# Performance work log

Measured on AMD Instinct MI355X. Metric: run time of the kernel, lower is better.

The kernel has to match this reference:

```python
import jax, jax.numpy as jnp
import numpy as np

N_NODES = 100000
N_EDGES = 1600000
HID = 64
EDGE_DIM = 16
SC_DIM = 6  # max_cycle(8) - MIN_CYCLE(3) + 1
N_LAYERS = 2
MSG_IN = 2 * HID + 2 * SC_DIM + EDGE_DIM  # 156
UPD_IN = 2 * HID


def setup_inputs() -> dict:
    key = jax.random.key(0)
    ks = jax.random.split(key, 16)
    s = 0.05
    inp = {
        "x": jax.random.normal(ks[0], (N_NODES, HID), dtype=jnp.float32),
        "edge_list": jax.random.randint(ks[1], (N_EDGES, 2), 0, N_NODES, dtype=jnp.int32),
        "node_struct": jax.random.randint(ks[2], (N_NODES, SC_DIM), 0, 4, dtype=jnp.int32),
        "edge_feature": jax.random.normal(ks[3], (N_EDGES, EDGE_DIM), dtype=jnp.float32),
        "edge_weight": jnp.ones((N_EDGES,), dtype=jnp.float32),
        "node2graph": jnp.sort(jax.random.randint(ks[4], (N_NODES,), 0, 128, dtype=jnp.int32)),
        "num_graphs": 128,
        # params
        "lin_w": jax.random.normal(ks[5], (HID, HID), dtype=jnp.float32) * s,
        "lin_b": jnp.zeros((HID,), dtype=jnp.float32),
        "msg_w1": jax.random.normal(ks[6], (N_LAYERS, MSG_IN, HID), dtype=jnp.float32) * s,
        "msg_b1": jnp.zeros((N_LAYERS, HID), dtype=jnp.float32),
        "msg_w2": jax.random.normal(ks[7], (N_LAYERS, HID, HID), dtype=jnp.float32) * s,
        "msg_b2": jnp.zeros((N_LAYERS, HID), dtype=jnp.float32),
        "upd_w1": jax.random.normal(ks[8], (N_LAYERS, UPD_IN, HID), dtype=jnp.float32) * s,
        "upd_b1": jnp.zeros((N_LAYERS, HID), dtype=jnp.float32),
        "upd_w2": jax.random.normal(ks[9], (N_LAYERS, HID, HID), dtype=jnp.float32) * s,
        "upd_b2": jnp.zeros((N_LAYERS, HID), dtype=jnp.float32),
    }
    return inp


def reference(x, edge_list, node_struct, edge_feature, edge_weight, node2graph,
              num_graphs, lin_w, lin_b, msg_w1, msg_b1, msg_w2, msg_b2,
              upd_w1, upd_b1, upd_w2, upd_b2):
    n_node = x.shape[0]
    src = edge_list[:, 0]
    dst = edge_list[:, 1]
    sc = node_struct.astype(x.dtype)          # [N, 6] structural cycle counts
    h = x @ lin_w + lin_b                      # input projection [N, HID]
    for l in range(N_LAYERS):
        # message: gather endpoints + structural feats + edge feats, 2-layer MLP
        m = jnp.concatenate([h[src], h[dst], sc[src], sc[dst], edge_feature], axis=-1)
        m = jax.nn.relu(m @ msg_w1[l] + msg_b1[l]) @ msg_w2[l] + msg_b2[l]
        # aggregate: weighted scatter_add onto destination nodes
        upd = jax.ops.segment_sum(m * edge_weight[:, None], dst, num_segments=n_node)
        # combine: cat(input, update) -> 2-layer MLP -> outer activation
        z = jnp.concatenate([h, upd], axis=-1)
        z = jax.nn.relu(z @ upd_w1[l] + upd_b1[l]) @ upd_w2[l] + upd_b2[l]
        h = jax.nn.relu(z)
    node_feature = h
    graph_feature = jax.ops.segment_sum(node_feature, node2graph, num_segments=num_graphs)
    return graph_feature, node_feature
```

## Files before the change

### kernel.cpp

```cpp
#include <hip/hip_runtime.h>

#define NN 100000
#define NE 1600000
#define HID 64
#define MSG_IN 156
#define W1E_OFF 140

__device__ __forceinline__ void mm4x4(float (&acc)[4][4], const float4 a, const float4 b) {
    acc[0][0] = fmaf(a.x, b.x, acc[0][0]);
    acc[0][1] = fmaf(a.x, b.y, acc[0][1]);
    acc[0][2] = fmaf(a.x, b.z, acc[0][2]);
    acc[0][3] = fmaf(a.x, b.w, acc[0][3]);
    acc[1][0] = fmaf(a.y, b.x, acc[1][0]);
    acc[1][1] = fmaf(a.y, b.y, acc[1][1]);
    acc[1][2] = fmaf(a.y, b.z, acc[1][2]);
    acc[1][3] = fmaf(a.y, b.w, acc[1][3]);
    acc[2][0] = fmaf(a.z, b.x, acc[2][0]);
    acc[2][1] = fmaf(a.z, b.y, acc[2][1]);
    acc[2][2] = fmaf(a.z, b.z, acc[2][2]);
    acc[2][3] = fmaf(a.z, b.w, acc[2][3]);
    acc[3][0] = fmaf(a.w, b.x, acc[3][0]);
    acc[3][1] = fmaf(a.w, b.y, acc[3][1]);
    acc[3][2] = fmaf(a.w, b.z, acc[3][2]);
    acc[3][3] = fmaf(a.w, b.w, acc[3][3]);
}


__global__ __launch_bounds__(256) void k_sw(
    const int2* __restrict__ el2, const float* __restrict__ ew,
    float* __restrict__ sw, int n_edges)
{
    int e = blockIdx.x * 256 + threadIdx.x;
    if (e < n_edges) atomicAdd(&sw[el2[e].y], ew[e]);
}

__global__ __launch_bounds__(256) void k_hist2(
    const int2* __restrict__ el2, const float* __restrict__ ew,
    int* __restrict__ counts, float* __restrict__ sw, int n_edges)
{
    int e = blockIdx.x * 256 + threadIdx.x;
    if (e < n_edges) {
        int2 sd = el2[e];
        atomicAdd(&counts[sd.y], 1);
        atomicAdd(&sw[sd.y], ew[e]);
    }
}

__global__ __launch_bounds__(256) void k_scan1(
    const int* counts, int* offs, int* __restrict__ blksum, int n)
{
    __shared__ int s[256];
    const int tid = threadIdx.x;
    int i = blockIdx.x * 256 + tid;
    int v = (i < n) ? counts[i] : 0;
    s[tid] = v;
    for (int off = 1; off < 256; off <<= 1) {
        __syncthreads();
        int t = (tid >= off) ? s[tid - off] : 0;
        __syncthreads();
        s[tid] += t;
    }
    __syncthreads();
    if (i < n) offs[i] = s[tid] - v;
    if (tid == 255) blksum[blockIdx.x] = s[255];
}

__global__ __launch_bounds__(512) void k_scan2(int* __restrict__ blksum, int nb)
{
    __shared__ int s[512];
    const int tid = threadIdx.x;
    int v = (tid < nb) ? blksum[tid] : 0;
    s[tid] = v;
    for (int off = 1; off < 512; off <<= 1) {
        __syncthreads();
        int t = (tid >= off) ? s[tid - off] : 0;
        __syncthreads();
        s[tid] += t;
    }
    __syncthreads();
    if (tid < nb) blksum[tid] = s[tid] - v;
}

__global__ __launch_bounds__(256) void k_scan3(
    int* __restrict__ offs, const int* __restrict__ blksum, int n)
{
    int i = blockIdx.x * 256 + threadIdx.x;
    if (i < n) offs[i] += blksum[blockIdx.x];
}

__global__ __launch_bounds__(256) void k_permute(
    const int2* __restrict__ el2, int* __restrict__ cursor,
    int* __restrict__ perm, int n_edges)
{
    int e = blockIdx.x * 256 + threadIdx.x;
    if (e < n_edges) {
        int pos = atomicAdd(&cursor[el2[e].y], 1);
        perm[pos] = e;
    }
}

__global__ __launch_bounds__(256) void k_csmall(
    const float* __restrict__ msg_w2, const float* __restrict__ upd_w1,
    const float* __restrict__ msg_b2, float* __restrict__ C2, float* __restrict__ db2)
{
    const int l = blockIdx.x;
    const float* W2  = msg_w2 + (size_t)l * 4096;
    const float* U1b = upd_w1 + (size_t)l * 8192 + 4096;
    const float* b2  = msg_b2 + l * 64;
    float* C  = C2  + (size_t)l * 4096;
    float* db = db2 + l * 64;
    __shared__ __align__(16) float At[64][68];
    __shared__ __align__(16) float B[64][64];
    const int tid = threadIdx.x;
    for (int i = tid; i < 1024; i += 256) {
        ((float4*)B)[i] = ((const float4*)U1b)[i];
        int m = i >> 4, f4 = i & 15, k4 = f4 * 4;
        float4 v = ((const float4*)W2)[m * 16 + f4];
        At[k4 + 0][m] = v.x; At[k4 + 1][m] = v.y; At[k4 + 2][m] = v.z; At[k4 + 3][m] = v.w;
    }
    __syncthreads();
    const int ty = tid >> 4, tx = tid & 15;
    float acc[4][4];
    #pragma unroll
    for (int r = 0; r < 4; ++r) { acc[r][0]=0.f; acc[r][1]=0.f; acc[r][2]=0.f; acc[r][3]=0.f; }
    #pragma unroll 8
    for (int k = 0; k < 64; ++k) {
        float4 a = *(const float4*)&At[k][ty * 4];
        float4 bv = *(const float4*)&B[k][tx * 4];
        mm4x4(acc, a, bv);
    }
    #pragma unroll
    for (int r = 0; r < 4; ++r)
        ((float4*)C)[(ty * 4 + r) * 16 + tx] = make_float4(acc[r][0], acc[r][1], acc[r][2], acc[r][3]);
    if (tid < 64) {
        float sum = 0.f;
        for (int k = 0; k < 64; ++k) sum += b2[k] * B[k][tid];
        db[tid] = sum;
    }
}


__global__ __launch_bounds__(256) void k_init(
    const float* __restrict__ x, const float* __restrict__ w,
    const float* __restrict__ b, float* __restrict__ h, int n)
{
    __shared__ __align__(16) float At[64][68];
    __shared__ __align__(16) float B[64][64];
    const int tid = threadIdx.x;
    const int m0 = blockIdx.x * 64;
    for (int i = tid; i < 1024; i += 256)
        ((float4*)B)[i] = ((const float4*)w)[i];
    for (int i = tid; i < 1024; i += 256) {
        int m = i >> 4, f4 = i & 15, k4 = f4 * 4;
        int node = m0 + m;
        float4 v = make_float4(0.f, 0.f, 0.f, 0.f);
        if (node < n) v = ((const float4*)x)[node * 16 + f4];
        At[k4 + 0][m] = v.x; At[k4 + 1][m] = v.y; At[k4 + 2][m] = v.z; At[k4 + 3][m] = v.w;
    }
    __syncthreads();
    const int ty = tid >> 4, tx = tid & 15;
    float acc[4][4];
    {
        float4 bb = ((const float4*)b)[tx];
        #pragma unroll
        for (int r = 0; r < 4; ++r) { acc[r][0]=bb.x; acc[r][1]=bb.y; acc[r][2]=bb.z; acc[r][3]=bb.w; }
    }
    #pragma unroll 8
    for (int k = 0; k < 64; ++k) {
        float4 a = *(const float4*)&At[k][ty * 4];
        float4 bv = *(const float4*)&B[k][tx * 4];
        mm4x4(acc, a, bv);
    }
    #pragma unroll
    for (int r = 0; r < 4; ++r) {
        int node = m0 + ty * 4 + r;
        if (node < n)
            ((float4*)h)[node * 16 + tx] = make_float4(acc[r][0], acc[r][1], acc[r][2], acc[r][3]);
    }
}

__global__ __launch_bounds__(256) void k_pq(
    const float* __restrict__ h, const int* __restrict__ nsc,
    const float* __restrict__ w1, const float* __restrict__ b1,
    float* __restrict__ p, float* __restrict__ q, int n)
{
    __shared__ __align__(16) float At[64][68];
    __shared__ __align__(16) float Bp[64][64];
    __shared__ __align__(16) float Bq[64][64];
    __shared__ __align__(16) float Sct[6][68];
    __shared__ __align__(16) float Bc[6][64];
    __shared__ __align__(16) float Bd[6][64];
    const int tid = threadIdx.x;
    const int m0 = blockIdx.x * 64;
    for (int i = tid; i < 1024; i += 256) {
        ((float4*)Bp)[i] = ((const float4*)w1)[i];
        ((float4*)Bq)[i] = ((const float4*)(w1 + 64 * 64))[i];
    }
    if (tid < 96) {
        ((float4*)Bc)[tid] = ((const float4*)(w1 + 128 * 64))[tid];
        ((float4*)Bd)[tid] = ((const float4*)(w1 + 134 * 64))[tid];
    }
    for (int i = tid; i < 1024; i += 256) {
        int m = i >> 4, f4 = i & 15, k4 = f4 * 4;
        int node = m0 + m;
        float4 v = make_float4(0.f, 0.f, 0.f, 0.f);
        if (node < n) v = ((const float4*)h)[node * 16 + f4];
        At[k4 + 0][m] = v.x; At[k4 + 1][m] = v.y; At[k4 + 2][m] = v.z; At[k4 + 3][m] = v.w;
    }
    for (int i = tid; i < 384; i += 256) {
        int m = i & 63, k = i >> 6;
        int node = m0 + m;
        float v = 0.f;
        if (node < n) v = (float)nsc[node * 6 + k];
        Sct[k][m] = v;
    }
    __syncthreads();
    const int ty = tid >> 4, tx = tid & 15;
    float ap[4][4], aq[4][4];
    {
        float4 bb = ((const float4*)b1)[tx];
        #pragma unroll
        for (int r = 0; r < 4; ++r) {
            ap[r][0]=0.f; ap[r][1]=0.f; ap[r][2]=0.f; ap[r][3]=0.f;
            aq[r][0]=bb.x; aq[r][1]=bb.y; aq[r][2]=bb.z; aq[r][3]=bb.w;
        }
    }
    #pragma unroll 8
    for (int k = 0; k < 64; ++k) {
        float4 a  = *(const float4*)&At[k][ty * 4];
        float4 bp = *(const float4*)&Bp[k][tx * 4];
        float4 bq = *(const float4*)&Bq[k][tx * 4];
        mm4x4(ap, a, bp);
        mm4x4(aq, a, bq);
    }
    #pragma unroll
    for (int k = 0; k < 6; ++k) {
        float4 a  = *(const float4*)&Sct[k][ty * 4];
        float4 bc = *(const float4*)&Bc[k][tx * 4];
        float4 bd = *(const float4*)&Bd[k][tx * 4];
        mm4x4(ap, a, bc);
        mm4x4(aq, a, bd);
    }
    #pragma unroll
    for (int r = 0; r < 4; ++r) {
        int node = m0 + ty * 4 + r;
        if (node < n) {
            ((float4*)p)[node * 16 + tx] = make_float4(ap[r][0], ap[r][1], ap[r][2], ap[r][3]);
            ((float4*)q)[node * 16 + tx] = make_float4(aq[r][0], aq[r][1], aq[r][2], aq[r][3]);
        }
    }
}


struct Meta { int pe[4]; };
struct El   { int s[4]; int d[4]; float w[4]; };
struct Pv   { float4 pv[4]; };
struct Run  { int d; float s0, s1, s2, s3; };

__device__ __forceinline__ void load_perm(Meta& m, int& spe, int c0, int eEnd,
    int ty, int tid, const int* __restrict__ perm)
{
    #pragma unroll
    for (int r = 0; r < 4; ++r) {
        int e = c0 + ty * 4 + r;
        m.pe[r] = perm[e < eEnd ? e : (eEnd - 1)];
    }
    int es = c0 + (tid >> 2);
    spe = perm[es < eEnd ? es : (eEnd - 1)];
}

__device__ __forceinline__ void load_el(El& e, const Meta& m,
    const int2* __restrict__ el2, const float* __restrict__ ew)
{
    #pragma unroll
    for (int r = 0; r < 4; ++r) {
        int2 sd = el2[m.pe[r]];
        e.s[r] = sd.x; e.d[r] = sd.y; e.w[r] = ew[m.pe[r]];
    }
}

__device__ __forceinline__ void load_p(Pv& z, const El& e,
    const float4* __restrict__ p4, int tx)
{
    #pragma unroll
    for (int r = 0; r < 4; ++r)
        z.pv[r] = p4[(size_t)e.s[r] * 16 + tx];
}

__device__ __forceinline__ void stage_ef(float (*Eb)[68], float4 v, int tid)
{
    int e = tid >> 2, k4 = (tid & 3) * 4;
    Eb[k4 + 0][e] = v.x; Eb[k4 + 1][e] = v.y;
    Eb[k4 + 2][e] = v.z; Eb[k4 + 3][e] = v.w;
}

__device__ __forceinline__ void flush_run(float (*Sacc)[68], const Run& run,
    int d0, int tx)
{
    float* dp = &Sacc[run.d - d0][tx * 4];
    atomicAdd(dp + 0, run.s0); atomicAdd(dp + 1, run.s1);
    atomicAdd(dp + 2, run.s2); atomicAdd(dp + 3, run.s3);
}

__device__ __forceinline__ void compute_chunk(const El& el, const Pv& pvr,
    int c0, int eEnd, int d0, const float (*Eb)[68], const float (*W1e)[64],
    float (*Sacc)[68], const float4* __restrict__ q4, int ty, int tx, Run& run)
{
    float4 qv[4];
    #pragma unroll
    for (int r = 0; r < 4; ++r)
        qv[r] = q4[(size_t)el.d[r] * 16 + tx];
    float acc[4][4];
    #pragma unroll
    for (int r = 0; r < 4; ++r) {
        acc[r][0] = pvr.pv[r].x; acc[r][1] = pvr.pv[r].y;
        acc[r][2] = pvr.pv[r].z; acc[r][3] = pvr.pv[r].w;
    }
    #pragma unroll
    for (int k = 0; k < 16; ++k) {
        float4 a = *(const float4*)&Eb[k][ty * 4];
        float4 bv = *(const float4*)&W1e[k][tx * 4];
        mm4x4(acc, a, bv);
    }
    #pragma unroll
    for (int r = 0; r < 4; ++r) {
        acc[r][0] += qv[r].x; acc[r][1] += qv[r].y;
        acc[r][2] += qv[r].z; acc[r][3] += qv[r].w;
    }
    #pragma unroll
    for (int r = 0; r < 4; ++r) {
        bool act = (c0 + ty * 4 + r) < eEnd;
        float w = act ? el.w[r] : 0.f;
        int d = el.d[r];
        float v0 = fmaxf(acc[r][0], 0.f) * w;
        float v1 = fmaxf(acc[r][1], 0.f) * w;
        float v2 = fmaxf(acc[r][2], 0.f) * w;
        float v3 = fmaxf(acc[r][3], 0.f) * w;
        if (d != run.d) {
            if (run.d >= 0) flush_run(Sacc, run, d0, tx);
            run.d = d; run.s0 = v0; run.s1 = v1; run.s2 = v2; run.s3 = v3;
        } else {
            run.s0 += v0; run.s1 += v1; run.s2 += v2; run.s3 += v3;
        }
    }
}

__device__ __forceinline__ void step(int c0, int eEnd, int d0, int& buf,
    Meta& mX, int& speX, El& elX, Pv& pvX,
    Meta& mY, int& speY, El& elY, Pv& pvY,
    const int* __restrict__ perm, const int2* __restrict__ el2,
    const float* __restrict__ ew, const float4* __restrict__ ef4,
    const float4* __restrict__ p4, const float4* __restrict__ q4,
    float (*Et)[16][68], const float (*W1e)[64], float (*Sacc)[68],
    int tid, int ty, int tx, Run& run)
{
    float4 efv = ef4[(size_t)speY * 4 + (tid & 3)];
    load_p(pvY, elY, p4, tx);
    load_perm(mX, speX, c0 + 128, eEnd, ty, tid, perm);
    compute_chunk(elX, pvX, c0, eEnd, d0, Et[buf], W1e, Sacc, q4, ty, tx, run);
    load_el(elX, mX, el2, ew);
    stage_ef(Et[buf ^ 1], efv, tid);
    __syncthreads();
    buf ^= 1;
}

__global__ __launch_bounds__(256) void k_edge5(
    const int* __restrict__ perm, const int* __restrict__ ends,
    const int2* __restrict__ el2, const float* __restrict__ ew,
    const float* __restrict__ ef,
    const float* __restrict__ p, const float* __restrict__ q,
    const float* __restrict__ w1e, float* __restrict__ S, int n_nodes)
{
    __shared__ __align__(16) float W1e[16][64];
    __shared__ __align__(16) float Sacc[64][68];
    __shared__ __align__(16) float Et[2][16][68];
    const int tid = threadIdx.x;
    int b = blockIdx.x;
    {
        const int nb = gridDim.x;
        const int qn = nb >> 3, rr = nb & 7;
        const int xcd = b & 7, idx = b >> 3;
        b = (xcd < rr ? xcd * (qn + 1) : rr * (qn + 1) + (xcd - rr) * qn) + idx;
    }
    const int d0 = b * 64;
    const int dn = min(64, n_nodes - d0);
    const int eStart = (d0 == 0) ? 0 : ends[d0 - 1];
    const int eEnd   = ends[d0 + dn - 1];
    const int nc = (eEnd - eStart + 63) >> 6;

    const float4* p4  = (const float4*)p;
    const float4* q4  = (const float4*)q;
    const float4* ef4 = (const float4*)ef;

    ((float4*)W1e)[tid] = ((const float4*)w1e)[tid];
    for (int i = tid; i < 64 * 17; i += 256)
        ((float4*)Sacc)[i] = make_float4(0.f, 0.f, 0.f, 0.f);

    const int ty = tid >> 4, tx = tid & 15;
    Run run; run.d = -1; run.s0 = run.s1 = run.s2 = run.s3 = 0.f;

    if (nc > 0) {
        Meta mX, mY; int speX, speY;
        El elX, elY;
        Pv pvX, pvY;
        load_perm(mX, speX, eStart, eEnd, ty, tid, perm);
        load_el(elX, mX, el2, ew);
        float4 ef0 = ef4[(size_t)speX * 4 + (tid & 3)];
        load_p(pvX, elX, p4, tx);
        load_perm(mY, speY, eStart + 64, eEnd, ty, tid, perm);
        load_el(elY, mY, el2, ew);
        stage_ef(Et[0], ef0, tid);
        __syncthreads();

        int buf = 0;
        for (int c = 0; c < nc; c += 2) {
            step(eStart + (c << 6), eEnd, d0, buf,
                 mX, speX, elX, pvX, mY, speY, elY, pvY,
                 perm, el2, ew, ef4, p4, q4, Et, W1e, Sacc, tid, ty, tx, run);
            if (c + 1 < nc)
                step(eStart + ((c + 1) << 6), eEnd, d0, buf,
                     mY, speY, elY, pvY, mX, speX, elX, pvX,
                     perm, el2, ew, ef4, p4, q4, Et, W1e, Sacc, tid, ty, tx, run);
        }
    }
    if (run.d >= 0) flush_run(Sacc, run, d0, tx);
    __syncthreads();
    for (int i = tid; i < dn * 16; i += 256) {
        int row = i >> 4, f4 = i & 15;
        ((float4*)S)[(size_t)(d0 + row) * 16 + f4] = *(const float4*)&Sacc[row][f4 * 4];
    }
}

__global__ __launch_bounds__(256) void k_edge2(
    const int* __restrict__ perm, const int2* __restrict__ el2,
    const float* __restrict__ ew, const float* __restrict__ ef,
    const float* __restrict__ p, const float* __restrict__ q,
    const float* __restrict__ w1e, float* __restrict__ S, int n_edges)
{
    __shared__ __align__(16) float Et[16][68];
    __shared__ __align__(16) float W1e[16][64];
    __shared__ int Ssrc[64];
    __shared__ int Sdst[64];
    __shared__ float Sew[64];
    const int tid = threadIdx.x;
    const int b = blockIdx.x, nb = gridDim.x;
    const int tile = ((nb & 7) == 0) ? ((b & 7) * (nb >> 3) + (b >> 3)) : b;
    const int e0 = tile * 64;
    if (tid < 64) {
        int e = e0 + tid;
        int s = 0, d = 0; float w = 0.f;
        if (e < n_edges) {
            int pe = perm ? perm[e] : e;
            int2 sd = el2[pe];
            s = sd.x; d = sd.y; w = ew[pe];
        }
        Ssrc[tid] = s; Sdst[tid] = d; Sew[tid] = w;
    }
    ((float4*)W1e)[tid] = ((const float4*)w1e)[tid];
    {
        int e = tid >> 2, f4 = tid & 3, k4 = f4 * 4;
        int ge = e0 + e;
        float4 v = make_float4(0.f, 0.f, 0.f, 0.f);
        if (ge < n_edges) {
            int pe = perm ? perm[ge] : ge;
            v = ((const float4*)ef)[(size_t)pe * 4 + f4];
        }
        Et[k4 + 0][e] = v.x; Et[k4 + 1][e] = v.y; Et[k4 + 2][e] = v.z; Et[k4 + 3][e] = v.w;
    }
    __syncthreads();
    const int ty = tid >> 4, tx = tid & 15;
    float acc[4][4];
    #pragma unroll
    for (int r = 0; r < 4; ++r) {
        int s = Ssrc[ty * 4 + r], d = Sdst[ty * 4 + r];
        float4 pv = ((const float4*)p)[(size_t)s * 16 + tx];
        float4 qv = ((const float4*)q)[(size_t)d * 16 + tx];
        acc[r][0] = pv.x + qv.x; acc[r][1] = pv.y + qv.y;
        acc[r][2] = pv.z + qv.z; acc[r][3] = pv.w + qv.w;
    }
    #pragma unroll
    for (int k = 0; k < 16; ++k) {
        float4 a = *(const float4*)&Et[k][ty * 4];
        float4 bv = *(const float4*)&W1e[k][tx * 4];
        mm4x4(acc, a, bv);
    }
    {
        int curd = -1;
        float s0 = 0.f, s1 = 0.f, s2 = 0.f, s3 = 0.f;
        #pragma unroll
        for (int r = 0; r < 4; ++r) {
            int le = ty * 4 + r;
            int ge = e0 + le;
            if (ge < n_edges) {
                int d = Sdst[le];
                float w = Sew[le];
                float v0 = fmaxf(acc[r][0], 0.f) * w;
                float v1 = fmaxf(acc[r][1], 0.f) * w;
                float v2 = fmaxf(acc[r][2], 0.f) * w;
                float v3 = fmaxf(acc[r][3], 0.f) * w;
                if (d != curd) {
                    if (curd >= 0) {
                        atomicAdd(&S[(size_t)curd * 64 + tx * 4 + 0], s0);
                        atomicAdd(&S[(size_t)curd * 64 + tx * 4 + 1], s1);
                        atomicAdd(&S[(size_t)curd * 64 + tx * 4 + 2], s2);
                        atomicAdd(&S[(size_t)curd * 64 + tx * 4 + 3], s3);
                    }
                    curd = d; s0 = v0; s1 = v1; s2 = v2; s3 = v3;
                } else {
                    s0 += v0; s1 += v1; s2 += v2; s3 += v3;
                }
            }
        }
        if (curd >= 0) {
            atomicAdd(&S[(size_t)curd * 64 + tx * 4 + 0], s0);
            atomicAdd(&S[(size_t)curd * 64 + tx * 4 + 1], s1);
            atomicAdd(&S[(size_t)curd * 64 + tx * 4 + 2], s2);
            atomicAdd(&S[(size_t)curd * 64 + tx * 4 + 3], s3);
        }
    }
}

__global__ __launch_bounds__(256) void k_update(
    float* __restrict__ h, const float* __restrict__ S,
    const float* __restrict__ w1, const float* __restrict__ C,
    const float* __restrict__ b1, const float* __restrict__ w2,
    const float* __restrict__ b2, const float* __restrict__ db,
    const float* __restrict__ sw,
    int n, int write_out, float* __restrict__ out_graph,
    const int* __restrict__ n2g)
{
    __shared__ __align__(16) float At[64][68];
    __shared__ __align__(16) float B1[128][64];
    __shared__ float Db[64];
    const int tid = threadIdx.x;
    const int m0 = blockIdx.x * 64;
    const int ty = tid >> 4, tx = tid & 15;
    if (tid < 64) Db[tid] = db[tid];
    for (int i = tid; i < 2048; i += 256)
        ((float4*)B1)[i] = (i < 1024) ? ((const float4*)w1)[i] : ((const float4*)C)[i - 1024];
    for (int i = tid; i < 1024; i += 256) {
        int m = i >> 4, f4 = i & 15, k4 = f4 * 4;
        int node = m0 + m;
        float4 v = make_float4(0.f, 0.f, 0.f, 0.f);
        if (node < n) v = ((const float4*)h)[node * 16 + f4];
        At[k4 + 0][m] = v.x; At[k4 + 1][m] = v.y; At[k4 + 2][m] = v.z; At[k4 + 3][m] = v.w;
    }
    __syncthreads();
    float acc[4][4];
    {
        float4 bb = ((const float4*)b1)[tx];
        #pragma unroll
        for (int r = 0; r < 4; ++r) { acc[r][0]=bb.x; acc[r][1]=bb.y; acc[r][2]=bb.z; acc[r][3]=bb.w; }
    }
    #pragma unroll 8
    for (int k = 0; k < 64; ++k) {
        float4 a = *(const float4*)&At[k][ty * 4];
        float4 bv = *(const float4*)&B1[k][tx * 4];
        mm4x4(acc, a, bv);
    }
    __syncthreads();
    for (int i = tid; i < 1024; i += 256) {
        int m = i >> 4, f4 = i & 15, k4 = f4 * 4;
        int node = m0 + m;
        float4 v = make_float4(0.f, 0.f, 0.f, 0.f);
        if (node < n) v = ((const float4*)S)[node * 16 + f4];
        At[k4 + 0][m] = v.x; At[k4 + 1][m] = v.y; At[k4 + 2][m] = v.z; At[k4 + 3][m] = v.w;
    }
    __syncthreads();
    #pragma unroll 8
    for (int k = 0; k < 64; ++k) {
        float4 a = *(const float4*)&At[k][ty * 4];
        float4 bv = *(const float4*)&B1[64 + k][tx * 4];
        mm4x4(acc, a, bv);
    }
    #pragma unroll
    for (int r = 0; r < 4; ++r) {
        int node = m0 + ty * 4 + r;
        float swv = (node < n) ? sw[node] : 0.f;
        #pragma unroll
        for (int c = 0; c < 4; ++c)
            acc[r][c] = fmaf(swv, Db[tx * 4 + c], acc[r][c]);
    }
    __syncthreads();
    #pragma unroll
    for (int r = 0; r < 4; ++r)
        #pragma unroll
        for (int c = 0; c < 4; ++c)
            At[tx * 4 + c][ty * 4 + r] = fmaxf(acc[r][c], 0.f);
    for (int i = tid; i < 1024; i += 256)
        ((float4*)B1)[i] = ((const float4*)w2)[i];
    __syncthreads();
    float acc2[4][4];
    {
        float4 bb = ((const float4*)b2)[tx];
        #pragma unroll
        for (int r = 0; r < 4; ++r) { acc2[r][0]=bb.x; acc2[r][1]=bb.y; acc2[r][2]=bb.z; acc2[r][3]=bb.w; }
    }
    #pragma unroll 8
    for (int k = 0; k < 64; ++k) {
        float4 a = *(const float4*)&At[k][ty * 4];
        float4 bv = *(const float4*)&B1[k][tx * 4];
        mm4x4(acc2, a, bv);
    }
    float hv[4][4];
    #pragma unroll
    for (int r = 0; r < 4; ++r)
        #pragma unroll
        for (int c = 0; c < 4; ++c)
            hv[r][c] = fmaxf(acc2[r][c], 0.f);
    #pragma unroll
    for (int r = 0; r < 4; ++r) {
        int node = m0 + ty * 4 + r;
        if (node < n)
            ((float4*)h)[node * 16 + tx] = make_float4(hv[r][0], hv[r][1], hv[r][2], hv[r][3]);
    }
    if (write_out) {
        int curg = -1;
        float s0 = 0.f, s1 = 0.f, s2 = 0.f, s3 = 0.f;
        #pragma unroll
        for (int r = 0; r < 4; ++r) {
            int node = m0 + ty * 4 + r;
            if (node < n) {
                int g = n2g[node];
                if (g != curg) {
                    if (curg >= 0) {
                        atomicAdd(&out_graph[curg * 64 + tx * 4 + 0], s0);
                        atomicAdd(&out_graph[curg * 64 + tx * 4 + 1], s1);
                        atomicAdd(&out_graph[curg * 64 + tx * 4 + 2], s2);
                        atomicAdd(&out_graph[curg * 64 + tx * 4 + 3], s3);
                    }
                    curg = g; s0 = hv[r][0]; s1 = hv[r][1]; s2 = hv[r][2]; s3 = hv[r][3];
                } else {
                    s0 += hv[r][0]; s1 += hv[r][1]; s2 += hv[r][2]; s3 += hv[r][3];
                }
            }
        }
        if (curg >= 0) {
            atomicAdd(&out_graph[curg * 64 + tx * 4 + 0], s0);
            atomicAdd(&out_graph[curg * 64 + tx * 4 + 1], s1);
            atomicAdd(&out_graph[curg * 64 + tx * 4 + 2], s2);
            atomicAdd(&out_graph[curg * 64 + tx * 4 + 3], s3);
        }
    }
}

extern "C" void kernel_launch(void* const* d_in, const int* in_sizes, int n_in,
                              void* d_out, int out_size, void* d_ws, size_t ws_size,
                              hipStream_t stream)
{
    const float* x       = (const float*)d_in[0];
    const int2*  el2     = (const int2*)d_in[1];
    const int*   nsc     = (const int*)d_in[2];
    const float* ef      = (const float*)d_in[3];
    const float* ew      = (const float*)d_in[4];
    const int*   n2g     = (const int*)d_in[5];
    const float* lin_w   = (const float*)d_in[7];
    const float* lin_b   = (const float*)d_in[8];
    const float* msg_w1  = (const float*)d_in[9];
    const float* msg_b1  = (const float*)d_in[10];
    const float* msg_w2  = (const float*)d_in[11];
    const float* upd_w1  = (const float*)d_in[13];
    const float* upd_b1  = (const float*)d_in[14];
    const float* upd_w2  = (const float*)d_in[15];
    const float* upd_b2  = (const float*)d_in[16];
    const float* msg_b2  = (const float*)d_in[12];

    float* out_graph = (float*)d_out;
    float* h   = (float*)d_out + 128 * 64;

    const size_t NNH = (size_t)NN * HID;
    float* p  = (float*)d_ws;
    float* q  = p + NNH;
    float* S  = q + NNH;
    char*  cur = (char*)(S + NNH);
    const size_t base   = 3 * NNH * sizeof(float);
    const size_t szPerm = (size_t)NE * sizeof(int);
    const size_t szCnt  = (size_t)NN * sizeof(int);
    const size_t szSw   = (size_t)NN * sizeof(float);
    const size_t szBlk  = 4096;
    const size_t szC    = 2 * 64 * 64 * sizeof(float);
    const size_t szDb   = 2 * 64 * sizeof(float);
    const size_t need_sort = base + szPerm + szCnt + szBlk + szSw + szC + szDb;

    int *perm = nullptr, *counts = nullptr, *blksum = nullptr;
    float *sw, *C2, *db2;
    const int do_sort = (ws_size >= need_sort) ? 1 : 0;
    if (do_sort) {
        perm   = (int*)cur;        cur += szPerm;
        counts = (int*)cur;        cur += szCnt;
        blksum = (int*)cur;        cur += szBlk;
    }
    sw  = (float*)cur;             cur += szSw;
    C2  = (float*)cur;             cur += szC;
    db2 = (float*)cur;

    const int nblk_n  = (NN + 63) / 64;
    const int nblk_e  = (NE + 63) / 64;
    const int nblk_eh = (NE + 255) / 256;
    const int nblk_sc = (NN + 255) / 256;

    hipMemsetAsync(d_out, 0, 128 * 64 * sizeof(float), stream);
    hipMemsetAsync(sw, 0, szSw, stream);

    if (do_sort) {
        hipMemsetAsync(counts, 0, szCnt, stream);
        k_hist2<<<nblk_eh, 256, 0, stream>>>(el2, ew, counts, sw, NE);
        k_scan1<<<nblk_sc, 256, 0, stream>>>(counts, counts, blksum, NN);
        k_scan2<<<1, 512, 0, stream>>>(blksum, nblk_sc);
        k_scan3<<<nblk_sc, 256, 0, stream>>>(counts, blksum, NN);
        k_permute<<<nblk_eh, 256, 0, stream>>>(el2, counts, perm, NE);
    } else {
        k_sw<<<nblk_eh, 256, 0, stream>>>(el2, ew, sw, NE);
    }
    k_csmall<<<2, 256, 0, stream>>>(msg_w2, upd_w1, msg_b2, C2, db2);

    k_init<<<nblk_n, 256, 0, stream>>>(x, lin_w, lin_b, h, NN);
    for (int l = 0; l < 2; ++l) {
        const float* w1 = msg_w1 + (size_t)l * MSG_IN * HID;
        k_pq<<<nblk_n, 256, 0, stream>>>(h, nsc, w1, msg_b1 + l * HID, p, q, NN);
        if (do_sort) {
            k_edge5<<<nblk_n, 256, 0, stream>>>(perm, counts, el2, ew, ef, p, q,
                                                w1 + W1E_OFF * HID, S, NN);
        } else {
            hipMemsetAsync(S, 0, NNH * sizeof(float), stream);
            k_edge2<<<nblk_e, 256, 0, stream>>>(nullptr, el2, ew, ef, p, q,
                                                w1 + W1E_OFF * HID, S, NE);
        }
        k_update<<<nblk_n, 256, 0, stream>>>(h, S,
                                             upd_w1 + (size_t)l * 2 * HID * HID,
                                             C2 + (size_t)l * 4096,
                                             upd_b1 + l * HID,
                                             upd_w2 + (size_t)l * HID * HID,
                                             upd_b2 + l * HID,
                                             db2 + l * 64, sw,
                                             NN, (l == 1) ? 1 : 0, out_graph, n2g);
    }
}
```

Before: 1.186 ms.

## Shrink sorted edge kernel to single-wave blocks over 16 destination nodes

The dst-sorted edge-message kernel now runs as one 64-thread wavefront per block covering 16 destination nodes and 16-edge chunks, instead of 256 threads over 64 nodes. Because each block is a single wave, the block-wide __syncthreads calls become wave barriers, and shared-memory staging and accumulators shrink. The aim is finer-grained load balancing across skewed node degrees, more resident blocks, and no cross-wave synchronisation stalls. In exchange each block reloads the 16x64 edge-weight slice, so there are about four times as many blocks paying setup and prologue costs.

Result: slower. 3.727 ms (+214.2%).

```diff
diff --git a/kernel.cpp b/kernel.cpp
--- a/kernel.cpp
+++ b/kernel.cpp
@@ -5,6 +5,7 @@
 #define HID 64
 #define MSG_IN 156
 #define W1E_OFF 140
+#define DPB 16
 
 __device__ __forceinline__ void mm4x4(float (&acc)[4][4], const float4 a, const float4 b) {
     acc[0][0] = fmaf(a.x, b.x, acc[0][0]);
@@ -257,7 +258,7 @@
 struct Pv   { float4 pv[4]; };
 struct Run  { int d; float s0, s1, s2, s3; };
 
-__device__ __forceinline__ void load_perm(Meta& m, int& spe, int c0, int eEnd,
+__device__ __forceinline__ void load_perm16(Meta& m, int& spe, int c0, int eEnd,
     int ty, int tid, const int* __restrict__ perm)
 {
     #pragma unroll
@@ -269,7 +270,7 @@
     spe = perm[es < eEnd ? es : (eEnd - 1)];
 }
 
-__device__ __forceinline__ void load_el(El& e, const Meta& m,
+__device__ __forceinline__ void load_el16(El& e, const Meta& m,
     const int2* __restrict__ el2, const float* __restrict__ ew)
 {
     #pragma unroll
@@ -279,7 +280,7 @@
     }
 }
 
-__device__ __forceinline__ void load_p(Pv& z, const El& e,
+__device__ __forceinline__ void load_p16(Pv& z, const El& e,
     const float4* __restrict__ p4, int tx)
 {
     #pragma unroll
@@ -287,14 +288,14 @@
         z.pv[r] = p4[(size_t)e.s[r] * 16 + tx];
 }
 
-__device__ __forceinline__ void stage_ef(float (*Eb)[68], float4 v, int tid)
+__device__ __forceinline__ void stage_ef16(float (*Eb)[20], float4 v, int tid)
 {
     int e = tid >> 2, k4 = (tid & 3) * 4;
     Eb[k4 + 0][e] = v.x; Eb[k4 + 1][e] = v.y;
     Eb[k4 + 2][e] = v.z; Eb[k4 + 3][e] = v.w;
 }
 
-__device__ __forceinline__ void flush_run(float (*Sacc)[68], const Run& run,
+__device__ __forceinline__ void flush_run16(float (*Sacc)[68], const Run& run,
     int d0, int tx)
 {
     float* dp = &Sacc[run.d - d0][tx * 4];
@@ -302,8 +303,8 @@
     atomicAdd(dp + 2, run.s2); atomicAdd(dp + 3, run.s3);
 }
 
-__device__ __forceinline__ void compute_chunk(const El& el, const Pv& pvr,
-    int c0, int eEnd, int d0, const float (*Eb)[68], const float (*W1e)[64],
+__device__ __forceinline__ void compute16(const El& el, const Pv& pvr,
+    int c0, int eEnd, int d0, const float (*Eb)[20], const float (*W1e)[64],
     float (*Sacc)[68], const float4* __restrict__ q4, int ty, int tx, Run& run)
 {
     float4 qv[4];
@@ -337,7 +338,7 @@
         float v2 = fmaxf(acc[r][2], 0.f) * w;
         float v3 = fmaxf(acc[r][3], 0.f) * w;
         if (d != run.d) {
-            if (run.d >= 0) flush_run(Sacc, run, d0, tx);
+            if (run.d >= 0) flush_run16(Sacc, run, d0, tx);
             run.d = d; run.s0 = v0; run.s1 = v1; run.s2 = v2; run.s3 = v3;
         } else {
             run.s0 += v0; run.s1 += v1; run.s2 += v2; run.s3 += v3;
@@ -345,26 +346,26 @@
     }
 }
 
-__device__ __forceinline__ void step(int c0, int eEnd, int d0, int& buf,
+__device__ __forceinline__ void step16(int c0, int eEnd, int d0, int& buf,
     Meta& mX, int& speX, El& elX, Pv& pvX,
     Meta& mY, int& speY, El& elY, Pv& pvY,
     const int* __restrict__ perm, const int2* __restrict__ el2,
     const float* __restrict__ ew, const float4* __restrict__ ef4,
     const float4* __restrict__ p4, const float4* __restrict__ q4,
-    float (*Et)[16][68], const float (*W1e)[64], float (*Sacc)[68],
+    float (*Et)[16][20], const float (*W1e)[64], float (*Sacc)[68],
     int tid, int ty, int tx, Run& run)
 {
     float4 efv = ef4[(size_t)speY * 4 + (tid & 3)];
-    load_p(pvY, elY, p4, tx);
-    load_perm(mX, speX, c0 + 128, eEnd, ty, tid, perm);
-    compute_chunk(elX, pvX, c0, eEnd, d0, Et[buf], W1e, Sacc, q4, ty, tx, run);
-    load_el(elX, mX, el2, ew);
-    stage_ef(Et[buf ^ 1], efv, tid);
-    __syncthreads();
+    load_p16(pvY, elY, p4, tx);
+    load_perm16(mX, speX, c0 + 32, eEnd, ty, tid, perm);
+    compute16(elX, pvX, c0, eEnd, d0, Et[buf], W1e, Sacc, q4, ty, tx, run);
+    load_el16(elX, mX, el2, ew);
+    stage_ef16(Et[buf ^ 1], efv, tid);
+    __builtin_amdgcn_wave_barrier();
     buf ^= 1;
 }
 
-__global__ __launch_bounds__(256) void k_edge5(
+__global__ __launch_bounds__(64, 4) void k_edge6(
     const int* __restrict__ perm, const int* __restrict__ ends,
     const int2* __restrict__ el2, const float* __restrict__ ew,
     const float* __restrict__ ef,
@@ -372,8 +373,8 @@
     const float* __restrict__ w1e, float* __restrict__ S, int n_nodes)
 {
     __shared__ __align__(16) float W1e[16][64];
-    __shared__ __align__(16) float Sacc[64][68];
-    __shared__ __align__(16) float Et[2][16][68];
+    __shared__ __align__(16) float Sacc[16][68];
+    __shared__ __align__(16) float Et[2][16][20];
     const int tid = threadIdx.x;
     int b = blockIdx.x;
     {
@@ -382,18 +383,19 @@
         const int xcd = b & 7, idx = b >> 3;
         b = (xcd < rr ? xcd * (qn + 1) : rr * (qn + 1) + (xcd - rr) * qn) + idx;
     }
-    const int d0 = b * 64;
-    const int dn = min(64, n_nodes - d0);
+    const int d0 = b * DPB;
+    const int dn = min(DPB, n_nodes - d0);
     const int eStart = (d0 == 0) ? 0 : ends[d0 - 1];
     const int eEnd   = ends[d0 + dn - 1];
-    const int nc = (eEnd - eStart + 63) >> 6;
+    const int nc = (eEnd - eStart + 15) >> 4;
 
     const float4* p4  = (const float4*)p;
     const float4* q4  = (const float4*)q;
     const float4* ef4 = (const float4*)ef;
 
-    ((float4*)W1e)[tid] = ((const float4*)w1e)[tid];
-    for (int i = tid; i < 64 * 17; i += 256)
+    for (int i = tid; i < 256; i += 64)
+        ((float4*)W1e)[i] = ((const float4*)w1e)[i];
+    for (int i = tid; i < 16 * 17; i += 64)
         ((float4*)Sacc)[i] = make_float4(0.f, 0.f, 0.f, 0.f);
 
     const int ty = tid >> 4, tx = tid & 15;
@@ -403,29 +405,29 @@
         Meta mX, mY; int speX, speY;
         El elX, elY;
         Pv pvX, pvY;
-        load_perm(mX, speX, eStart, eEnd, ty, tid, perm);
-        load_el(elX, mX, el2, ew);
+        load_perm16(mX, speX, eStart, eEnd, ty, tid, perm);
+        load_el16(elX, mX, el2, ew);
         float4 ef0 = ef4[(size_t)speX * 4 + (tid & 3)];
-        load_p(pvX, elX, p4, tx);
-        load_perm(mY, speY, eStart + 64, eEnd, ty, tid, perm);
-        load_el(elY, mY, el2, ew);
-        stage_ef(Et[0], ef0, tid);
-        __syncthreads();
+        load_p16(pvX, elX, p4, tx);
+        load_perm16(mY, speY, eStart + 16, eEnd, ty, tid, perm);
+        load_el16(elY, mY, el2, ew);
+        stage_ef16(Et[0], ef0, tid);
+        __builtin_amdgcn_wave_barrier();
 
         int buf = 0;
         for (int c = 0; c < nc; c += 2) {
-            step(eStart + (c << 6), eEnd, d0, buf,
-                 mX, speX, elX, pvX, mY, speY, elY, pvY,
-                 perm, el2, ew, ef4, p4, q4, Et, W1e, Sacc, tid, ty, tx, run);
+            step16(eStart + (c << 4), eEnd, d0, buf,
+                   mX, speX, elX, pvX, mY, speY, elY, pvY,
+                   perm, el2, ew, ef4, p4, q4, Et, W1e, Sacc, tid, ty, tx, run);
             if (c + 1 < nc)
-                step(eStart + ((c + 1) << 6), eEnd, d0, buf,
-                     mY, speY, elY, pvY, mX, speX, elX, pvX,
-                     perm, el2, ew, ef4, p4, q4, Et, W1e, Sacc, tid, ty, tx, run);
-        }
-    }
-    if (run.d >= 0) flush_run(Sacc, run, d0, tx);
-    __syncthreads();
-    for (int i = tid; i < dn * 16; i += 256) {
+                step16(eStart + ((c + 1) << 4), eEnd, d0, buf,
+                       mY, speY, elY, pvY, mX, speX, elX, pvX,
+                       perm, el2, ew, ef4, p4, q4, Et, W1e, Sacc, tid, ty, tx, run);
+        }
+    }
+    if (run.d >= 0) flush_run16(Sacc, run, d0, tx);
+    __builtin_amdgcn_wave_barrier();
+    for (int i = tid; i < dn * 16; i += 64) {
         int row = i >> 4, f4 = i & 15;
         ((float4*)S)[(size_t)(d0 + row) * 16 + f4] = *(const float4*)&Sacc[row][f4 * 4];
     }
@@ -695,6 +697,7 @@
     db2 = (float*)cur;
 
     const int nblk_n  = (NN + 63) / 64;
+    const int nblk_e6 = (NN + DPB - 1) / DPB;
     const int nblk_e  = (NE + 63) / 64;
     const int nblk_eh = (NE + 255) / 256;
     const int nblk_sc = (NN + 255) / 256;
@@ -719,7 +722,7 @@
         const float* w1 = msg_w1 + (size_t)l * MSG_IN * HID;
         k_pq<<<nblk_n, 256, 0, stream>>>(h, nsc, w1, msg_b1 + l * HID, p, q, NN);
         if (do_sort) {
-            k_edge5<<<nblk_n, 256, 0, stream>>>(perm, counts, el2, ew, ef, p, q,
+            k_edge6<<<nblk_e6, 64, 0, stream>>>(perm, counts, el2, ew, ef, p, q,
                                                 w1 + W1E_OFF * HID, S, NN);
         } else {
             hipMemsetAsync(S, 0, NNH * sizeof(float), stream);
```
